# Optimization experiments

Measured on AMD Instinct MI355X. Metric: run time of the kernel, lower is better.

Reference implementation:

```python
import jax, jax.numpy as jnp
import numpy as np

N, L, G, NB = 1024, 30, 10000, 64  # cells, latent, genes, n_batch

def setup_inputs() -> dict:
    key = jax.random.key(0)
    k = jax.random.split(key, 7)
    z = jax.random.normal(k[0], (N, L), dtype=jnp.float32)
    batch_covariate = jax.random.randint(k[1], (N,), 0, NB, dtype=jnp.int32)
    size_factor = jax.random.uniform(k[2], (N, 1), dtype=jnp.float32)
    # learned params
    W_amat = jax.random.normal(k[3], (L, G), dtype=jnp.float32) * 0.05   # Dense(n_out, use_bias=False)
    A_emb = jax.random.normal(k[4], (NB, G, L), dtype=jnp.float32) * 0.05  # Embed(n_batch, n_out*n_in)
    b_emb = jax.random.normal(k[5], (NB, G), dtype=jnp.float32) * 0.05     # Embed(n_batch, n_out)
    px_r = jax.random.normal(k[6], (G,), dtype=jnp.float32)                # param 'px_r'
    return {"z": z, "batch_covariate": batch_covariate, "size_factor": size_factor,
            "W_amat": W_amat, "A_emb": A_emb, "b_emb": b_emb, "px_r": px_r}

def reference(z, batch_covariate, size_factor, W_amat, A_emb, b_emb, px_r):
    # h1 = Dense(n_out, no bias)(z)
    h1 = z @ W_amat                                  # [N, G]
    # dropout is deterministic (training=False) -> identity; stop_gradient as in source
    z_drop = jax.lax.stop_gradient(z)                # [N, L]
    idx = batch_covariate.astype(jnp.int32).reshape(-1)
    A_b = A_emb[idx]                                 # [N, G, L] per-sample gathered matrix
    h2 = jnp.einsum('cgl,cl->cg', A_b, z_drop)       # [N, G]
    h3 = b_emb[idx]                                  # [N, G]
    mu = jax.nn.softplus(h1 + h2 + h3)               # activation = nn.softplus
    mean = mu * size_factor                          # NegativeBinomial mean
    inverse_dispersion = jnp.exp(px_r)               # NegativeBinomial inverse_dispersion
    return mean, inverse_dispersion
```

## Files before the change

### kernel.cpp

```cpp
#include <hip/hip_runtime.h>

#define NCELLS 1024
#define LDIM   30
#define GDIM   10000
#define NBATCH 64
#define GPB    256
#define CELLCAP 256

typedef unsigned int u32;

#define GLOBAL_AS __attribute__((address_space(1)))
#define LDS_AS    __attribute__((address_space(3)))

__global__ __launch_bounds__(256, 5) void decoder_kernel(
    const float* __restrict__ z,
    const void*  __restrict__ cand1,
    const void*  __restrict__ cand2,
    const float* __restrict__ W,
    const float* __restrict__ A,
    const float* __restrict__ Bb,
    const float* __restrict__ px,
    float* __restrict__ out)
{
    const int b   = blockIdx.x;
    const int tid = threadIdx.x;
    const int gb  = blockIdx.y * GPB;
    const int g   = gb + tid;
    const int gc  = g < GDIM ? g : GDIM - 1;

    __shared__ __align__(16) float a_sh[GPB * LDIM];
    __shared__ int cells[CELLCAP];
    __shared__ int cnt;

    if (tid == 0) cnt = 0;
    __syncthreads();

    const size_t abase = ((size_t)b * GDIM + gb) * LDIM;
    const size_t atot  = (size_t)NBATCH * GDIM * LDIM;
    {
        const int wbase = __builtin_amdgcn_readfirstlane(tid);
        #pragma unroll
        for (int k = 0; k < 8; k++) {
            const int i4 = k * 256 + tid;
            if (i4 < GPB * LDIM / 4) {
                const size_t gidx = abase + (size_t)i4 * 4;
                if (gidx + 4 <= atot) {
                    __builtin_amdgcn_global_load_lds(
                        (const GLOBAL_AS void*)(A + gidx),
                        (LDS_AS void*)(a_sh + (size_t)(k * 256 + wbase) * 4),
                        16, 0, 0);
                }
            }
        }
    }

    const u32 probe = ((const u32*)cand1)[tid & 63];
    const bool c1_is_int = __all(probe < 64u);
    const int*   bcov = c1_is_int ? (const int*)cand1   : (const int*)cand2;
    const float* sf   = c1_is_int ? (const float*)cand2 : (const float*)cand1;

    for (int i = tid; i < NCELLS; i += 256) {
        if (bcov[i] == b) {
            int p = atomicAdd(&cnt, 1);
            if (p < CELLCAP) cells[p] = i;
        }
    }

    float m[LDIM];
    #pragma unroll
    for (int l = 0; l < LDIM; l++) m[l] = W[(size_t)l * GDIM + gc];
    const float h3 = Bb[(size_t)b * GDIM + gc];

    __syncthreads();

    if (g >= GDIM) return;

    {
        const float2* ar = (const float2*)(a_sh + tid * LDIM);
        #pragma unroll
        for (int j = 0; j < LDIM / 2; j++) {
            float2 w = ar[j];
            m[2 * j]     += w.x;
            m[2 * j + 1] += w.y;
        }
    }

    if (b == 0) out[(size_t)NCELLS * GDIM + g] = __expf(px[g]);

    const int total = cnt < CELLCAP ? cnt : CELLCAP;
    int id0 = cells[0];
    int id1 = cells[1];
    int c = 0;
    for (; c + 2 <= total; c += 2) {
        const int cell0 = __builtin_amdgcn_readfirstlane(id0);
        const int cell1 = __builtin_amdgcn_readfirstlane(id1);
        const int n0 = (c + 2 < total) ? c + 2 : 0;
        const int n1 = (c + 3 < total) ? c + 3 : 0;
        id0 = cells[n0];
        id1 = cells[n1];
        const float* z0 = z + (size_t)cell0 * LDIM;
        const float* z1 = z + (size_t)cell1 * LDIM;
        const float s0 = sf[cell0], s1 = sf[cell1];
        float a0 = h3, b0 = 0.f, a1 = h3, b1 = 0.f;
        #pragma unroll
        for (int l = 0; l < LDIM; l += 2) {
            a0 = fmaf(m[l],     z0[l],     a0);
            b0 = fmaf(m[l + 1], z0[l + 1], b0);
            a1 = fmaf(m[l],     z1[l],     a1);
            b1 = fmaf(m[l + 1], z1[l + 1], b1);
        }
        float x0 = a0 + b0, x1 = a1 + b1;
        float p0 = fmaxf(x0, 0.f) + __logf(1.f + __expf(-fabsf(x0)));
        float p1 = fmaxf(x1, 0.f) + __logf(1.f + __expf(-fabsf(x1)));
        __builtin_nontemporal_store(p0 * s0, &out[(size_t)cell0 * GDIM + g]);
        __builtin_nontemporal_store(p1 * s1, &out[(size_t)cell1 * GDIM + g]);
    }
    if (c < total) {
        const int cell0 = __builtin_amdgcn_readfirstlane(id0);
        const float* z0 = z + (size_t)cell0 * LDIM;
        const float s0 = sf[cell0];
        float a0 = h3, b0 = 0.f;
        #pragma unroll
        for (int l = 0; l < LDIM; l += 2) {
            a0 = fmaf(m[l],     z0[l],     a0);
            b0 = fmaf(m[l + 1], z0[l + 1], b0);
        }
        float x0 = a0 + b0;
        float p0 = fmaxf(x0, 0.f) + __logf(1.f + __expf(-fabsf(x0)));
        __builtin_nontemporal_store(p0 * s0, &out[(size_t)cell0 * GDIM + g]);
    }
}

extern "C" void kernel_launch(void* const* d_in, const int* in_sizes, int n_in,
                              void* d_out, int out_size, void* d_ws, size_t ws_size,
                              hipStream_t stream) {
    const float* z  = nullptr;
    const float* W  = nullptr;
    const float* A  = nullptr;
    const float* Bb = nullptr;
    const float* px = nullptr;
    const void*  p1024[2] = {nullptr, nullptr};
    int n1024 = 0;
    for (int i = 0; i < n_in; i++) {
        switch (in_sizes[i]) {
            case NCELLS * LDIM:        z  = (const float*)d_in[i]; break;
            case LDIM * GDIM:          W  = (const float*)d_in[i]; break;
            case NBATCH * GDIM * LDIM: A  = (const float*)d_in[i]; break;
            case NBATCH * GDIM:        Bb = (const float*)d_in[i]; break;
            case GDIM:                 px = (const float*)d_in[i]; break;
            case NCELLS:
                if (n1024 < 2) p1024[n1024] = d_in[i];
                n1024++;
                break;
            default: break;
        }
    }
    if (!z || !W || !A || !Bb || !px || n1024 != 2) {
        z  = (const float*)d_in[0];
        p1024[0] = d_in[1];
        p1024[1] = d_in[2];
        W  = (const float*)d_in[3];
        A  = (const float*)d_in[4];
        Bb = (const float*)d_in[5];
        px = (const float*)d_in[6];
    }
    float* out = (float*)d_out;

    decoder_kernel<<<dim3(NBATCH, (GDIM + GPB - 1) / GPB), 256, 0, stream>>>(
        z, p1024[0], p1024[1], W, A, Bb, px, out);
}
```

Baseline: 156.1 us.

## Replace block-wide LDS cell list with per-wave ballot scan and readlane

Each wave now builds its own list of cells for the batch with ballot and popcount instead of shared atomics plus block barriers. It keeps cell ids and size factors in lane registers and reads them with readlane. The per-gene A row is read straight from global memory rather than staged through LDS, and the cell loop is unrolled by four. These changes remove both __syncthreads and the 30 KB LDS staging buffer so more blocks can be resident. In exchange, every wave rescans all 1024 covariates, each lane reads A in a strided pattern, and the per-wave list is capped at 64 cells.

```diff
diff --git a/kernel.cpp b/kernel.cpp
--- a/kernel.cpp
+++ b/kernel.cpp
@@ -5,14 +5,13 @@
 #define GDIM   10000
 #define NBATCH 64
 #define GPB    256
-#define CELLCAP 256
+#define WGENES 64
+#define WCAP   64
 
 typedef unsigned int u32;
+typedef unsigned long long u64;
 
-#define GLOBAL_AS __attribute__((address_space(1)))
-#define LDS_AS    __attribute__((address_space(3)))
-
-__global__ __launch_bounds__(256, 5) void decoder_kernel(
+__global__ __launch_bounds__(256, 6) void decoder_kernel(
     const float* __restrict__ z,
     const void*  __restrict__ cand1,
     const void*  __restrict__ cand2,
@@ -22,103 +21,97 @@
     const float* __restrict__ px,
     float* __restrict__ out)
 {
-    const int b   = blockIdx.x;
-    const int tid = threadIdx.x;
-    const int gb  = blockIdx.y * GPB;
-    const int g   = gb + tid;
-    const int gc  = g < GDIM ? g : GDIM - 1;
+    const int b    = blockIdx.x;
+    const int tid  = threadIdx.x;
+    const int lane = tid & 63;
+    const int wid  = __builtin_amdgcn_readfirstlane(tid >> 6);
+    const int g    = blockIdx.y * GPB + wid * WGENES + lane;
+    const bool valid = (g < GDIM);
+    const int gc   = valid ? g : GDIM - 1;
 
-    __shared__ __align__(16) float a_sh[GPB * LDIM];
-    __shared__ int cells[CELLCAP];
-    __shared__ int cnt;
+    __shared__ int wlist[4][WCAP];
 
-    if (tid == 0) cnt = 0;
-    __syncthreads();
-
-    const size_t abase = ((size_t)b * GDIM + gb) * LDIM;
-    const size_t atot  = (size_t)NBATCH * GDIM * LDIM;
-    {
-        const int wbase = __builtin_amdgcn_readfirstlane(tid);
-        #pragma unroll
-        for (int k = 0; k < 8; k++) {
-            const int i4 = k * 256 + tid;
-            if (i4 < GPB * LDIM / 4) {
-                const size_t gidx = abase + (size_t)i4 * 4;
-                if (gidx + 4 <= atot) {
-                    __builtin_amdgcn_global_load_lds(
-                        (const GLOBAL_AS void*)(A + gidx),
-                        (LDS_AS void*)(a_sh + (size_t)(k * 256 + wbase) * 4),
-                        16, 0, 0);
-                }
-            }
-        }
-    }
-
-    const u32 probe = ((const u32*)cand1)[tid & 63];
+    const u32 probe = ((const u32*)cand1)[lane];
     const bool c1_is_int = __all(probe < 64u);
     const int*   bcov = c1_is_int ? (const int*)cand1   : (const int*)cand2;
     const float* sf   = c1_is_int ? (const float*)cand2 : (const float*)cand1;
 
-    for (int i = tid; i < NCELLS; i += 256) {
-        if (bcov[i] == b) {
-            int p = atomicAdd(&cnt, 1);
-            if (p < CELLCAP) cells[p] = i;
+    float m[LDIM];
+    {
+        const float2* arow = (const float2*)(A + ((size_t)b * GDIM + gc) * LDIM);
+        #pragma unroll
+        for (int j = 0; j < LDIM / 2; j++) {
+            const float2 av = arow[j];
+            m[2 * j]     = W[(size_t)(2 * j)     * GDIM + gc] + av.x;
+            m[2 * j + 1] = W[(size_t)(2 * j + 1) * GDIM + gc] + av.y;
         }
     }
+    const float h3  = Bb[(size_t)b * GDIM + gc];
+    const float pxv = px[gc];
 
-    float m[LDIM];
-    #pragma unroll
-    for (int l = 0; l < LDIM; l++) m[l] = W[(size_t)l * GDIM + gc];
-    const float h3 = Bb[(size_t)b * GDIM + gc];
+    wlist[wid][lane] = 0;
+    int cnt = 0;
+    const u64 below = (1ull << lane) - 1ull;
+    for (int i0 = 0; i0 < NCELLS; i0 += 64) {
+        const int v = bcov[i0 + lane];
+        const u64 mb = __ballot(v == b);
+        if (v == b) {
+            const int pos = cnt + (int)__popcll(mb & below);
+            if (pos < WCAP) wlist[wid][pos] = i0 + lane;
+        }
+        cnt += (int)__popcll(mb);
+    }
+    const int total = cnt < WCAP ? cnt : WCAP;
 
-    __syncthreads();
+    int   myid = wlist[wid][lane];
+    float mysf = sf[myid];
+    asm volatile("" : "+v"(myid), "+v"(mysf));
 
-    if (g >= GDIM) return;
+    if (valid && b == 0) out[(size_t)NCELLS * GDIM + g] = __expf(pxv);
 
-    {
-        const float2* ar = (const float2*)(a_sh + tid * LDIM);
-        #pragma unroll
-        for (int j = 0; j < LDIM / 2; j++) {
-            float2 w = ar[j];
-            m[2 * j]     += w.x;
-            m[2 * j + 1] += w.y;
-        }
-    }
-
-    if (b == 0) out[(size_t)NCELLS * GDIM + g] = __expf(px[g]);
-
-    const int total = cnt < CELLCAP ? cnt : CELLCAP;
-    int id0 = cells[0];
-    int id1 = cells[1];
     int c = 0;
-    for (; c + 2 <= total; c += 2) {
-        const int cell0 = __builtin_amdgcn_readfirstlane(id0);
-        const int cell1 = __builtin_amdgcn_readfirstlane(id1);
-        const int n0 = (c + 2 < total) ? c + 2 : 0;
-        const int n1 = (c + 3 < total) ? c + 3 : 0;
-        id0 = cells[n0];
-        id1 = cells[n1];
+    for (; c + 4 <= total; c += 4) {
+        const int cell0 = __builtin_amdgcn_readlane(myid, c);
+        const int cell1 = __builtin_amdgcn_readlane(myid, c + 1);
+        const int cell2 = __builtin_amdgcn_readlane(myid, c + 2);
+        const int cell3 = __builtin_amdgcn_readlane(myid, c + 3);
+        const float s0 = __int_as_float(__builtin_amdgcn_readlane(__float_as_int(mysf), c));
+        const float s1 = __int_as_float(__builtin_amdgcn_readlane(__float_as_int(mysf), c + 1));
+        const float s2 = __int_as_float(__builtin_amdgcn_readlane(__float_as_int(mysf), c + 2));
+        const float s3 = __int_as_float(__builtin_amdgcn_readlane(__float_as_int(mysf), c + 3));
         const float* z0 = z + (size_t)cell0 * LDIM;
         const float* z1 = z + (size_t)cell1 * LDIM;
-        const float s0 = sf[cell0], s1 = sf[cell1];
+        const float* z2 = z + (size_t)cell2 * LDIM;
+        const float* z3 = z + (size_t)cell3 * LDIM;
         float a0 = h3, b0 = 0.f, a1 = h3, b1 = 0.f;
+        float a2 = h3, b2 = 0.f, a3 = h3, b3 = 0.f;
         #pragma unroll
         for (int l = 0; l < LDIM; l += 2) {
             a0 = fmaf(m[l],     z0[l],     a0);
             b0 = fmaf(m[l + 1], z0[l + 1], b0);
             a1 = fmaf(m[l],     z1[l],     a1);
             b1 = fmaf(m[l + 1], z1[l + 1], b1);
+            a2 = fmaf(m[l],     z2[l],     a2);
+            b2 = fmaf(m[l + 1], z2[l + 1], b2);
+            a3 = fmaf(m[l],     z3[l],     a3);
+            b3 = fmaf(m[l + 1], z3[l + 1], b3);
         }
-        float x0 = a0 + b0, x1 = a1 + b1;
+        float x0 = a0 + b0, x1 = a1 + b1, x2 = a2 + b2, x3 = a3 + b3;
         float p0 = fmaxf(x0, 0.f) + __logf(1.f + __expf(-fabsf(x0)));
         float p1 = fmaxf(x1, 0.f) + __logf(1.f + __expf(-fabsf(x1)));
-        __builtin_nontemporal_store(p0 * s0, &out[(size_t)cell0 * GDIM + g]);
-        __builtin_nontemporal_store(p1 * s1, &out[(size_t)cell1 * GDIM + g]);
+        float p2 = fmaxf(x2, 0.f) + __logf(1.f + __expf(-fabsf(x2)));
+        float p3 = fmaxf(x3, 0.f) + __logf(1.f + __expf(-fabsf(x3)));
+        if (valid) {
+            __builtin_nontemporal_store(p0 * s0, &out[(size_t)cell0 * GDIM + g]);
+            __builtin_nontemporal_store(p1 * s1, &out[(size_t)cell1 * GDIM + g]);
+            __builtin_nontemporal_store(p2 * s2, &out[(size_t)cell2 * GDIM + g]);
+            __builtin_nontemporal_store(p3 * s3, &out[(size_t)cell3 * GDIM + g]);
+        }
     }
-    if (c < total) {
-        const int cell0 = __builtin_amdgcn_readfirstlane(id0);
+    for (; c < total; c++) {
+        const int cell0 = __builtin_amdgcn_readlane(myid, c);
+        const float s0 = __int_as_float(__builtin_amdgcn_readlane(__float_as_int(mysf), c));
         const float* z0 = z + (size_t)cell0 * LDIM;
-        const float s0 = sf[cell0];
         float a0 = h3, b0 = 0.f;
         #pragma unroll
         for (int l = 0; l < LDIM; l += 2) {
@@ -127,7 +120,8 @@
         }
         float x0 = a0 + b0;
         float p0 = fmaxf(x0, 0.f) + __logf(1.f + __expf(-fabsf(x0)));
-        __builtin_nontemporal_store(p0 * s0, &out[(size_t)cell0 * GDIM + g]);
+        if (valid)
+            __builtin_nontemporal_store(p0 * s0, &out[(size_t)cell0 * GDIM + g]);
     }
 }
 
```

Result: slower. 175.0 us (+12.1%).
